# Kernel tuning notes

Measured on AMD Instinct MI355X. Metric: run time of the kernel, lower is better.

## Reference

```python
import jax, jax.numpy as jnp
import numpy as np

B, S, H = 2, 2048, 1024
NH, NKV, HD = 16, 4, 64
G, R = NKV, NH // NKV  # 4 kv groups, 4 query heads per group


def setup_inputs() -> dict:
    key = jax.random.key(0)
    ks = jax.random.split(key, 7)
    scale = 1.0 / np.sqrt(H)
    return {
        "hidden_states": jax.random.normal(ks[0], (B, S, H), jnp.float32),
        "cos": jax.random.normal(ks[1], (S, HD), jnp.float32),
        "sin": jax.random.normal(ks[2], (S, HD), jnp.float32),
        "attention_mask": jnp.ones((B, S), jnp.float32),
        "Wq": jax.random.normal(ks[3], (H, NH * HD), jnp.float32) * scale,
        "Wk": jax.random.normal(ks[4], (H, NKV * HD), jnp.float32) * scale,
        "Wv": jax.random.normal(ks[5], (H, NKV * HD), jnp.float32) * scale,
        "Wo": jax.random.normal(ks[6], (NH * HD, H), jnp.float32) * scale,
    }


def _rotate_half(x):
    h = x.shape[-1] // 2
    return jnp.concatenate([-x[..., h:], x[..., :h]], axis=-1)


def reference(hidden_states, cos, sin, attention_mask, Wq, Wk, Wv, Wo):
    x = hidden_states
    q = (x @ Wq).reshape(B, S, NH, HD)
    k = (x @ Wk).reshape(B, S, NKV, HD)
    v = (x @ Wv).reshape(B, S, NKV, HD)
    # RoPE: cos/sin [S,HD] broadcast over batch and heads
    c = cos[None, :, None, :]
    s = sin[None, :, None, :]
    q = q * c + _rotate_half(q) * s
    k = k * c + _rotate_half(k) * s
    # GQA without materializing repeated KV: q grouped as [B,S,G,R,HD]
    qg = q.reshape(B, S, G, R, HD)
    scores = jnp.einsum("bsgrd,btgd->bgrst", qg, k) / np.sqrt(HD)  # [B,G,R,S,T]
    causal = jnp.tril(jnp.ones((S, S), bool))
    scores = jnp.where(causal[None, None, None], scores, -jnp.inf)
    scores = scores + ((1.0 - attention_mask) * -1e9)[:, None, None, None, :]
    probs = jax.nn.softmax(scores.astype(jnp.float32), axis=-1).astype(q.dtype)
    out = jnp.einsum("bgrst,btgd->bsgrd", probs, v).reshape(B, S, NH * HD)
    return out @ Wo
```

## Files before the change

kernel.cpp:

```cpp
#include <hip/hip_runtime.h>
#include <math.h>

#define B_   2
#define S_   2048
#define H_   1024
#define NH_  16
#define NKV_ 4
#define HD_  64
#define R_   (NH_ / NKV_)
#define QKVW 1536

typedef __attribute__((ext_vector_type(8))) short bf16x8;
typedef __attribute__((ext_vector_type(4))) float f32x4;

__device__ inline short f2bf(float f) {
    unsigned u = __float_as_uint(f);
    u += 0x7FFF + ((u >> 16) & 1);
    return (short)(u >> 16);
}

__device__ inline void gload_lds16(const void* gptr, void* lptr) {
    __builtin_amdgcn_global_load_lds(
        (const __attribute__((address_space(1))) unsigned int*)gptr,
        (__attribute__((address_space(3))) unsigned int*)lptr,
        16, 0, 0);
}

__global__ __launch_bounds__(256) void tconv_all(const float* __restrict__ Wq,
                                                 const float* __restrict__ Wk,
                                                 const float* __restrict__ Wv,
                                                 const float* __restrict__ Wo,
                                                 short* __restrict__ Wqkvt,
                                                 short* __restrict__ Wot,
                                                 const float* __restrict__ x,
                                                 short* __restrict__ xb) {
    const int bx = blockIdx.x;
    const int tid = threadIdx.x;

    if (bx >= 640) {
        const size_t e0 = (size_t)(bx - 640) * 16384;
#pragma unroll
        for (int t = 0; t < 8; t++) {
            const size_t i = e0 + ((size_t)t * 256 + tid) * 8;
            float4 a = *(const float4*)&x[i];
            float4 c = *(const float4*)&x[i + 4];
            bf16x8 o;
            o[0] = f2bf(a.x); o[1] = f2bf(a.y); o[2] = f2bf(a.z); o[3] = f2bf(a.w);
            o[4] = f2bf(c.x); o[5] = f2bf(c.y); o[6] = f2bf(c.z); o[7] = f2bf(c.w);
            *(bf16x8*)&xb[i] = o;
        }
        return;
    }

    __shared__ short T[64][68];
    const float* W; short* Wt; int N, idx;
    if (bx < 256)      { W = Wq; Wt = Wqkvt;                     N = 1024; idx = bx; }
    else if (bx < 320) { W = Wk; Wt = Wqkvt + 1024 * 1024;       N = 256;  idx = bx - 256; }
    else if (bx < 384) { W = Wv; Wt = Wqkvt + 1280 * 1024;       N = 256;  idx = bx - 320; }
    else               { W = Wo; Wt = Wot;                       N = 1024; idx = bx - 384; }
    const int ntiles = N >> 6;
    const int n0 = (idx % ntiles) * 64;
    const int k0 = (idx / ntiles) * 64;

    const int r  = tid >> 4;
    const int c4 = (tid & 15) * 4;
#pragma unroll
    for (int t = 0; t < 4; t++) {
        int row = t * 16 + r;
        float4 v = *(const float4*)&W[(size_t)(k0 + row) * N + n0 + c4];
        T[c4 + 0][row] = f2bf(v.x);
        T[c4 + 1][row] = f2bf(v.y);
        T[c4 + 2][row] = f2bf(v.z);
        T[c4 + 3][row] = f2bf(v.w);
    }
    __syncthreads();
#pragma unroll
    for (int t = 0; t < 4; t++) {
        int row = t * 16 + r;
        short4 o = *(short4*)&T[row][c4];
        *(short4*)&Wt[(size_t)(n0 + row) * 1024 + k0 + c4] = o;
    }
}

__global__ __launch_bounds__(256) void gemm1_fused(const short* __restrict__ xb,
                                                   const short* __restrict__ Bt,
                                                   short* __restrict__ qkv,
                                                   short* __restrict__ Vtg,
                                                   const float* __restrict__ cosb,
                                                   const float* __restrict__ sinb) {
    __shared__ short Ah[128 * 32];
    __shared__ short Bh[128 * 32];

    const int tid  = threadIdx.x;
    const int w    = tid >> 6;
    const int lane = tid & 63;
    const int ln   = lane & 15;
    const int qd   = lane >> 4;
    const int wr   = w >> 1, wc = w & 1;
    const int row0 = blockIdx.y * 128;
    const int col0 = blockIdx.x * 128;

    const int sr = lane >> 2;
    const int sk = (lane & 3) * 8;

    f32x4 acc[4][4];
#pragma unroll
    for (int mi = 0; mi < 4; mi++)
#pragma unroll
        for (int ni = 0; ni < 4; ni++)
            acc[mi][ni] = (f32x4){0.f, 0.f, 0.f, 0.f};

    for (int k0 = 0; k0 < 1024; k0 += 32) {
        __syncthreads();
        gload_lds16(xb + (size_t)(row0 + w * 16 + sr) * 1024 + k0 + sk,      &Ah[(w * 16) * 32]);
        gload_lds16(xb + (size_t)(row0 + 64 + w * 16 + sr) * 1024 + k0 + sk, &Ah[(64 + w * 16) * 32]);
        gload_lds16(Bt + (size_t)(col0 + w * 16 + sr) * 1024 + k0 + sk,      &Bh[(w * 16) * 32]);
        gload_lds16(Bt + (size_t)(col0 + 64 + w * 16 + sr) * 1024 + k0 + sk, &Bh[(64 + w * 16) * 32]);
        __syncthreads();

        bf16x8 af[4], bf[4];
#pragma unroll
        for (int mi = 0; mi < 4; mi++)
            af[mi] = *(const bf16x8*)&Ah[(wr * 64 + mi * 16 + ln) * 32 + qd * 8];
#pragma unroll
        for (int ni = 0; ni < 4; ni++)
            bf[ni] = *(const bf16x8*)&Bh[(wc * 64 + ni * 16 + ln) * 32 + qd * 8];
#pragma unroll
        for (int mi = 0; mi < 4; mi++)
#pragma unroll
            for (int ni = 0; ni < 4; ni++)
                acc[mi][ni] = __builtin_amdgcn_mfma_f32_16x16x32_bf16(af[mi], bf[ni], acc[mi][ni], 0, 0, 0);
    }

    const int colw = col0 + wc * 64;
    if (colw < H_ + NKV_ * HD_) {
#pragma unroll
        for (int mi = 0; mi < 4; mi++)
#pragma unroll
            for (int i = 0; i < 4; i++) {
                const int row  = row0 + wr * 64 + mi * 16 + qd * 4 + i;
                const int spos = row & (S_ - 1);
                const float* cp = cosb + (size_t)spos * HD_;
                const float* sp = sinb + (size_t)spos * HD_;
                float o0[4];
#pragma unroll
                for (int ni = 0; ni < 2; ni++) {
                    const int d = ni * 16 + ln;
                    float x0 = acc[mi][ni][i], x1 = acc[mi][ni + 2][i];
                    o0[ni]     = x0 * cp[d]      - x1 * sp[d];
                    o0[ni + 2] = x1 * cp[d + 32] + x0 * sp[d + 32];
                }
                short* Cp = qkv + (size_t)row * QKVW + colw + ln;
#pragma unroll
                for (int ni = 0; ni < 4; ni++) Cp[ni * 16] = f2bf(o0[ni]);
            }
    } else {
        const int g = (colw - (H_ + NKV_ * HD_)) >> 6;
#pragma unroll
        for (int mi = 0; mi < 4; mi++) {
            const int rbase = row0 + wr * 64 + mi * 16 + qd * 4;
            const int bg = ((rbase >> 11) * NKV_) + g;
            const int s0 = rbase & (S_ - 1);
#pragma unroll
            for (int ni = 0; ni < 4; ni++) {
                const int d = ni * 16 + ln;
                short4 pk = { f2bf(acc[mi][ni][0]), f2bf(acc[mi][ni][1]),
                              f2bf(acc[mi][ni][2]), f2bf(acc[mi][ni][3]) };
                *(short4*)&Vtg[((size_t)bg * HD_ + d) * S_ + s0] = pk;
            }
        }
    }
}

__global__ __launch_bounds__(256) void gemm2_bt(const short* __restrict__ A, int lda,
                                                const short* __restrict__ Bt,
                                                float* __restrict__ C, int ldc,
                                                int K) {
    __shared__ short Ah[128 * 32];
    __shared__ short Bh[128 * 32];

    const int tid  = threadIdx.x;
    const int w    = tid >> 6;
    const int lane = tid & 63;
    const int ln   = lane & 15;
    const int qd   = lane >> 4;
    const int wr   = w >> 1, wc = w & 1;
    const int row0 = blockIdx.y * 128;
    const int col0 = blockIdx.x * 128;

    const int sr = lane >> 2;
    const int sk = (lane & 3) * 8;

    f32x4 acc[4][4];
#pragma unroll
    for (int mi = 0; mi < 4; mi++)
#pragma unroll
        for (int ni = 0; ni < 4; ni++)
            acc[mi][ni] = (f32x4){0.f, 0.f, 0.f, 0.f};

    for (int k0 = 0; k0 < K; k0 += 32) {
        __syncthreads();
        gload_lds16(A + (size_t)(row0 + w * 16 + sr) * lda + k0 + sk,      &Ah[(w * 16) * 32]);
        gload_lds16(A + (size_t)(row0 + 64 + w * 16 + sr) * lda + k0 + sk, &Ah[(64 + w * 16) * 32]);
        gload_lds16(Bt + (size_t)(col0 + w * 16 + sr) * K + k0 + sk,       &Bh[(w * 16) * 32]);
        gload_lds16(Bt + (size_t)(col0 + 64 + w * 16 + sr) * K + k0 + sk,  &Bh[(64 + w * 16) * 32]);
        __syncthreads();

        bf16x8 af[4], bf[4];
#pragma unroll
        for (int mi = 0; mi < 4; mi++)
            af[mi] = *(const bf16x8*)&Ah[(wr * 64 + mi * 16 + ln) * 32 + qd * 8];
#pragma unroll
        for (int ni = 0; ni < 4; ni++)
            bf[ni] = *(const bf16x8*)&Bh[(wc * 64 + ni * 16 + ln) * 32 + qd * 8];
#pragma unroll
        for (int mi = 0; mi < 4; mi++)
#pragma unroll
            for (int ni = 0; ni < 4; ni++)
                acc[mi][ni] = __builtin_amdgcn_mfma_f32_16x16x32_bf16(af[mi], bf[ni], acc[mi][ni], 0, 0, 0);
    }

#pragma unroll
    for (int mi = 0; mi < 4; mi++)
#pragma unroll
        for (int i = 0; i < 4; i++) {
            const size_t row = row0 + wr * 64 + mi * 16 + qd * 4 + i;
            float* Cp = C + row * ldc + col0 + wc * 64 + ln;
#pragma unroll
            for (int ni = 0; ni < 4; ni++) Cp[ni * 16] = acc[mi][ni][i];
        }
}

__global__ __launch_bounds__(512, 2) void attn_kernel(short* __restrict__ qkv,
                                                      const short* __restrict__ Vtg,
                                                      const float* __restrict__ maskb) {
    const int tid  = threadIdx.x;
    const int w    = tid >> 6;
    const int lane = tid & 63;
    const int ln   = lane & 15;
    const int qd   = lane >> 4;

    const int fid = blockIdx.x;
    const int bg  = fid & 7;
    const int u   = fid >> 3;
    const int b   = bg >> 2;
    const int g   = bg & 3;
    const int h   = g * R_ + (u & 3);
    const int a   = u >> 2;

    const int qt   = (w < 4) ? a : (15 - a);
    const int st   = w & 3;
    const int rowb = qt * 128 + st * 32;
    const int ktd  = 2 * qt + (st >> 1);
    const int nt   = 32 - 2 * a;

    __shared__ short Ks[2][64 * 72];
    __shared__ short Vt[2][64 * 72];
    __shared__ short Ps[8][16 * 72];
    __shared__ float mskS[2][64];
    short* const ps = Ps[w];

    const short* const Kb = qkv + (size_t)b * S_ * QKVW + H_ + g * HD_;
    const short* const Vb = Vtg + (size_t)bg * HD_ * S_;
    const float* const mb = maskb + b * S_;

    const int fr = tid >> 3;
    const int fc = (tid & 7) * 8;

    bf16x8 qf[2][2];
#pragma unroll
    for (int rg = 0; rg < 2; rg++) {
        const short* qp = qkv + (size_t)(b * S_ + rowb + rg * 16 + ln) * QKVW + h * HD_;
        qf[rg][0] = *(const bf16x8*)&qp[qd * 8];
        qf[rg][1] = *(const bf16x8*)&qp[32 + qd * 8];
    }

    f32x4 O[2][4] = {};
    float mrow[2] = {-1e30f, -1e30f};
    float lrow[2] = {0.0f, 0.0f};

    *(bf16x8*)&Ks[0][fr * 72 + fc] = *(const bf16x8*)&Kb[(size_t)fr * QKVW + fc];
    *(bf16x8*)&Vt[0][fr * 72 + fc] = *(const bf16x8*)&Vb[(size_t)fr * S_ + fc];
    if (tid < 64) mskS[0][tid] = mb[tid];
    __syncthreads();

    int cur = 0;
    for (int kt = 0; kt < nt; kt++) {
        const int base = kt * 64;
        const bool pf = (kt + 1 < nt);

        bf16x8 pk, pv;
        float pm = 0.0f;
        if (pf) {
            const int nb = base + 64;
            pk = *(const bf16x8*)&Kb[(size_t)(nb + fr) * QKVW + fc];
            pv = *(const bf16x8*)&Vb[(size_t)fr * S_ + nb + fc];
            if (tid < 64) pm = mb[nb + tid];
        }

        if (kt <= ktd) {
            f32x4 St[2][4];
#pragma unroll
            for (int kg = 0; kg < 4; kg++) {
                bf16x8 ka0 = *(const bf16x8*)&Ks[cur][(kg * 16 + ln) * 72 + qd * 8];
                bf16x8 ka1 = *(const bf16x8*)&Ks[cur][(kg * 16 + ln) * 72 + 32 + qd * 8];
#pragma unroll
                for (int rg = 0; rg < 2; rg++) {
                    f32x4 z = {0.f, 0.f, 0.f, 0.f};
                    z = __builtin_amdgcn_mfma_f32_16x16x32_bf16(ka0, qf[rg][0], z, 0, 0, 0);
                    St[rg][kg] = __builtin_amdgcn_mfma_f32_16x16x32_bf16(ka1, qf[rg][1], z, 0, 0, 0);
                }
            }

            bf16x8 vb[2][4];
#pragma unroll
            for (int kc2 = 0; kc2 < 2; kc2++)
#pragma unroll
                for (int dt = 0; dt < 4; dt++)
                    vb[kc2][dt] = *(const bf16x8*)&Vt[cur][(dt * 16 + ln) * 72 + kc2 * 32 + qd * 8];

            float mt[4][4];
#pragma unroll
            for (int kg = 0; kg < 4; kg++) {
                float4 mv = *(const float4*)&mskS[cur][kg * 16 + qd * 4];
                mt[kg][0] = (1.0f - mv.x) * -1e9f;
                mt[kg][1] = (1.0f - mv.y) * -1e9f;
                mt[kg][2] = (1.0f - mv.z) * -1e9f;
                mt[kg][3] = (1.0f - mv.w) * -1e9f;
            }

            const bool diag = (kt == ktd);

#pragma unroll
            for (int rg = 0; rg < 2; rg++) {
                const int qrow = rowb + rg * 16 + ln;
                float sc[4][4];
#pragma unroll
                for (int kg = 0; kg < 4; kg++) {
                    const int keyb = base + kg * 16 + qd * 4;
#pragma unroll
                    for (int i = 0; i < 4; i++) {
                        float v = fmaf(St[rg][kg][i], 0.125f, mt[kg][i]);
                        sc[kg][i] = (diag && (keyb + i > qrow)) ? -1e30f : v;
                    }
                }
                float mx = sc[0][0];
#pragma unroll
                for (int kg = 0; kg < 4; kg++)
#pragma unroll
                    for (int i = 0; i < 4; i++) mx = fmaxf(mx, sc[kg][i]);
                mx = fmaxf(mx, __shfl_xor(mx, 16));
                mx = fmaxf(mx, __shfl_xor(mx, 32));

                if (__ballot(mx > mrow[rg] + 8.0f)) {
                    float nm    = fmaxf(mrow[rg], mx);
                    float alpha = __expf(mrow[rg] - nm);
                    lrow[rg] *= alpha;
#pragma unroll
                    for (int i = 0; i < 4; i++) {
                        float av = __shfl(alpha, qd * 4 + i);
#pragma unroll
                        for (int dt = 0; dt < 4; dt++) O[rg][dt][i] *= av;
                    }
                    mrow[rg] = nm;
                }
                const float nm = mrow[rg];

                float ls = 0.0f;
#pragma unroll
                for (int kg = 0; kg < 4; kg++)
#pragma unroll
                    for (int i = 0; i < 4; i++) {
                        float p = __expf(sc[kg][i] - nm);
                        sc[kg][i] = p;
                        ls += p;
                    }
                ls += __shfl_xor(ls, 16);
                ls += __shfl_xor(ls, 32);
                lrow[rg] += ls;

#pragma unroll
                for (int kg = 0; kg < 4; kg++) {
                    short4 pk2 = { f2bf(sc[kg][0]), f2bf(sc[kg][1]),
                                   f2bf(sc[kg][2]), f2bf(sc[kg][3]) };
                    *(short4*)&ps[ln * 72 + kg * 16 + qd * 4] = pk2;
                }

#pragma unroll
                for (int kc2 = 0; kc2 < 2; kc2++) {
                    bf16x8 pa = *(const bf16x8*)&ps[ln * 72 + kc2 * 32 + qd * 8];
#pragma unroll
                    for (int dt = 0; dt < 4; dt++)
                        O[rg][dt] = __builtin_amdgcn_mfma_f32_16x16x32_bf16(pa, vb[kc2][dt], O[rg][dt], 0, 0, 0);
                }
            }
        }

        if (pf) {
            const int nxt = cur ^ 1;
            *(bf16x8*)&Ks[nxt][fr * 72 + fc] = pk;
            *(bf16x8*)&Vt[nxt][fr * 72 + fc] = pv;
            if (tid < 64) mskS[nxt][tid] = pm;
        }
        __syncthreads();
        cur ^= 1;
    }

#pragma unroll
    for (int rg = 0; rg < 2; rg++)
#pragma unroll
        for (int i = 0; i < 4; i++) {
            float li  = __shfl(lrow[rg], qd * 4 + i);
            float inv = 1.0f / li;
            const int row = rowb + rg * 16 + qd * 4 + i;
            short* op = qkv + (size_t)(b * S_ + row) * QKVW + h * HD_ + ln;
#pragma unroll
            for (int dt = 0; dt < 4; dt++) op[dt * 16] = f2bf(O[rg][dt][i] * inv);
        }
}

extern "C" void kernel_launch(void* const* d_in, const int* in_sizes, int n_in,
                              void* d_out, int out_size, void* d_ws, size_t ws_size,
                              hipStream_t stream) {
    const float* x     = (const float*)d_in[0];
    const float* cosb  = (const float*)d_in[1];
    const float* sinb  = (const float*)d_in[2];
    const float* maskb = (const float*)d_in[3];
    const float* Wq    = (const float*)d_in[4];
    const float* Wk    = (const float*)d_in[5];
    const float* Wv    = (const float*)d_in[6];
    const float* Wo    = (const float*)d_in[7];

    const int M = B_ * S_;

    short* qkv   = (short*)d_ws;
    short* Wqkvt = qkv + (size_t)M * QKVW;
    short* Wot   = Wqkvt + (size_t)QKVW * H_;
    short* Vtg   = Wot + (size_t)H_ * H_;
    short* xb    = (short*)d_out;
    float* out   = (float*)d_out;

    dim3 blk(256);

    tconv_all<<<dim3(896), blk, 0, stream>>>(Wq, Wk, Wv, Wo, Wqkvt, Wot, x, xb);

    gemm1_fused<<<dim3(QKVW / 128, M / 128), blk, 0, stream>>>(xb, Wqkvt, qkv, Vtg, cosb, sinb);

    attn_kernel<<<dim3(256), dim3(512), 0, stream>>>(qkv, Vtg, maskb);

    gemm2_bt<<<dim3(H_ / 128, M / 128), blk, 0, stream>>>(qkv, QKVW, Wot, out, H_, H_);
}
```

Before: 206.6 us.

## Process paired causal query tiles sequentially with all eight waves per tile

Before, each block split its eight waves into two groups, each handling a different query tile (a and 15-a) with 32 rows per wave, streaming K/V once across the longer range. Now all eight waves handle 16 rows each of one tile, then the block moves to the paired tile in a second phase, so each phase only streams the K/V range its tile needs. The mask transform is also precomputed when loading into shared memory. This halves per-wave register state and removes idle iterations for the short tile, but reloads K/V for the overlapping prefix and adds a second pipeline prologue and more barriers.

```diff
diff --git a/kernel.cpp b/kernel.cpp
--- a/kernel.cpp
+++ b/kernel.cpp
@@ -248,12 +248,6 @@
     const int h   = g * R_ + (u & 3);
     const int a   = u >> 2;
 
-    const int qt   = (w < 4) ? a : (15 - a);
-    const int st   = w & 3;
-    const int rowb = qt * 128 + st * 32;
-    const int ktd  = 2 * qt + (st >> 1);
-    const int nt   = 32 - 2 * a;
-
     __shared__ short Ks[2][64 * 72];
     __shared__ short Vt[2][64 * 72];
     __shared__ short Ps[8][16 * 72];
@@ -267,83 +261,81 @@
     const int fr = tid >> 3;
     const int fc = (tid & 7) * 8;
 
-    bf16x8 qf[2][2];
-#pragma unroll
-    for (int rg = 0; rg < 2; rg++) {
-        const short* qp = qkv + (size_t)(b * S_ + rowb + rg * 16 + ln) * QKVW + h * HD_;
-        qf[rg][0] = *(const bf16x8*)&qp[qd * 8];
-        qf[rg][1] = *(const bf16x8*)&qp[32 + qd * 8];
-    }
-
-    f32x4 O[2][4] = {};
-    float mrow[2] = {-1e30f, -1e30f};
-    float lrow[2] = {0.0f, 0.0f};
-
-    *(bf16x8*)&Ks[0][fr * 72 + fc] = *(const bf16x8*)&Kb[(size_t)fr * QKVW + fc];
-    *(bf16x8*)&Vt[0][fr * 72 + fc] = *(const bf16x8*)&Vb[(size_t)fr * S_ + fc];
-    if (tid < 64) mskS[0][tid] = mb[tid];
-    __syncthreads();
-
-    int cur = 0;
-    for (int kt = 0; kt < nt; kt++) {
-        const int base = kt * 64;
-        const bool pf = (kt + 1 < nt);
-
-        bf16x8 pk, pv;
-        float pm = 0.0f;
-        if (pf) {
-            const int nb = base + 64;
-            pk = *(const bf16x8*)&Kb[(size_t)(nb + fr) * QKVW + fc];
-            pv = *(const bf16x8*)&Vb[(size_t)fr * S_ + nb + fc];
-            if (tid < 64) pm = mb[nb + tid];
-        }
-
-        if (kt <= ktd) {
-            f32x4 St[2][4];
-#pragma unroll
-            for (int kg = 0; kg < 4; kg++) {
-                bf16x8 ka0 = *(const bf16x8*)&Ks[cur][(kg * 16 + ln) * 72 + qd * 8];
-                bf16x8 ka1 = *(const bf16x8*)&Ks[cur][(kg * 16 + ln) * 72 + 32 + qd * 8];
-#pragma unroll
-                for (int rg = 0; rg < 2; rg++) {
+#pragma unroll 1
+    for (int ph = 0; ph < 2; ph++) {
+        const int qt   = ph ? (15 - a) : a;
+        const int rowb = qt * 128 + w * 16;
+        const int ktd  = 2 * qt + (w >> 2);
+        const int ntp  = 2 * qt + 2;
+        const int qrow = rowb + ln;
+
+        bf16x8 qf0, qf1;
+        {
+            const short* qp = qkv + (size_t)(b * S_ + rowb + ln) * QKVW + h * HD_;
+            qf0 = *(const bf16x8*)&qp[qd * 8];
+            qf1 = *(const bf16x8*)&qp[32 + qd * 8];
+        }
+
+        f32x4 O[4] = {};
+        float mrow = -1e30f, lrow = 0.0f;
+
+        *(bf16x8*)&Ks[0][fr * 72 + fc] = *(const bf16x8*)&Kb[(size_t)fr * QKVW + fc];
+        *(bf16x8*)&Vt[0][fr * 72 + fc] = *(const bf16x8*)&Vb[(size_t)fr * S_ + fc];
+        if (tid < 64) mskS[0][tid] = (1.0f - mb[tid]) * -1e9f;
+        __syncthreads();
+
+        int cur = 0;
+#pragma unroll 1
+        for (int kt = 0; kt < ntp; kt++) {
+            const int base = kt * 64;
+            const bool pf = (kt + 1 < ntp);
+
+            bf16x8 pk, pv;
+            float pm = 0.0f;
+            if (pf) {
+                const int nb = base + 64;
+                pk = *(const bf16x8*)&Kb[(size_t)(nb + fr) * QKVW + fc];
+                pv = *(const bf16x8*)&Vb[(size_t)fr * S_ + nb + fc];
+                if (tid < 64) pm = (1.0f - mb[nb + tid]) * -1e9f;
+            }
+
+            if (kt <= ktd) {
+                f32x4 St[4];
+#pragma unroll
+                for (int kg = 0; kg < 4; kg++) {
+                    bf16x8 ka0 = *(const bf16x8*)&Ks[cur][(kg * 16 + ln) * 72 + qd * 8];
+                    bf16x8 ka1 = *(const bf16x8*)&Ks[cur][(kg * 16 + ln) * 72 + 32 + qd * 8];
                     f32x4 z = {0.f, 0.f, 0.f, 0.f};
-                    z = __builtin_amdgcn_mfma_f32_16x16x32_bf16(ka0, qf[rg][0], z, 0, 0, 0);
-                    St[rg][kg] = __builtin_amdgcn_mfma_f32_16x16x32_bf16(ka1, qf[rg][1], z, 0, 0, 0);
-                }
-            }
-
-            bf16x8 vb[2][4];
-#pragma unroll
-            for (int kc2 = 0; kc2 < 2; kc2++)
-#pragma unroll
-                for (int dt = 0; dt < 4; dt++)
-                    vb[kc2][dt] = *(const bf16x8*)&Vt[cur][(dt * 16 + ln) * 72 + kc2 * 32 + qd * 8];
-
-            float mt[4][4];
-#pragma unroll
-            for (int kg = 0; kg < 4; kg++) {
-                float4 mv = *(const float4*)&mskS[cur][kg * 16 + qd * 4];
-                mt[kg][0] = (1.0f - mv.x) * -1e9f;
-                mt[kg][1] = (1.0f - mv.y) * -1e9f;
-                mt[kg][2] = (1.0f - mv.z) * -1e9f;
-                mt[kg][3] = (1.0f - mv.w) * -1e9f;
-            }
-
-            const bool diag = (kt == ktd);
-
-#pragma unroll
-            for (int rg = 0; rg < 2; rg++) {
-                const int qrow = rowb + rg * 16 + ln;
+                    z = __builtin_amdgcn_mfma_f32_16x16x32_bf16(ka0, qf0, z, 0, 0, 0);
+                    St[kg] = __builtin_amdgcn_mfma_f32_16x16x32_bf16(ka1, qf1, z, 0, 0, 0);
+                }
+
+                bf16x8 vb[2][4];
+#pragma unroll
+                for (int kc2 = 0; kc2 < 2; kc2++)
+#pragma unroll
+                    for (int dt = 0; dt < 4; dt++)
+                        vb[kc2][dt] = *(const bf16x8*)&Vt[cur][(dt * 16 + ln) * 72 + kc2 * 32 + qd * 8];
+
                 float sc[4][4];
 #pragma unroll
                 for (int kg = 0; kg < 4; kg++) {
-                    const int keyb = base + kg * 16 + qd * 4;
-#pragma unroll
-                    for (int i = 0; i < 4; i++) {
-                        float v = fmaf(St[rg][kg][i], 0.125f, mt[kg][i]);
-                        sc[kg][i] = (diag && (keyb + i > qrow)) ? -1e30f : v;
+                    float4 mv = *(const float4*)&mskS[cur][kg * 16 + qd * 4];
+                    sc[kg][0] = fmaf(St[kg][0], 0.125f, mv.x);
+                    sc[kg][1] = fmaf(St[kg][1], 0.125f, mv.y);
+                    sc[kg][2] = fmaf(St[kg][2], 0.125f, mv.z);
+                    sc[kg][3] = fmaf(St[kg][3], 0.125f, mv.w);
+                }
+                if (kt == ktd) {
+#pragma unroll
+                    for (int kg = 0; kg < 4; kg++) {
+                        const int keyb = base + kg * 16 + qd * 4;
+#pragma unroll
+                        for (int i = 0; i < 4; i++)
+                            if (keyb + i > qrow) sc[kg][i] = -1e30f;
                     }
                 }
+
                 float mx = sc[0][0];
 #pragma unroll
                 for (int kg = 0; kg < 4; kg++)
@@ -352,19 +344,19 @@
                 mx = fmaxf(mx, __shfl_xor(mx, 16));
                 mx = fmaxf(mx, __shfl_xor(mx, 32));
 
-                if (__ballot(mx > mrow[rg] + 8.0f)) {
-                    float nm    = fmaxf(mrow[rg], mx);
-                    float alpha = __expf(mrow[rg] - nm);
-                    lrow[rg] *= alpha;
+                if (__ballot(mx > mrow + 8.0f)) {
+                    float nm    = fmaxf(mrow, mx);
+                    float alpha = __expf(mrow - nm);
+                    lrow *= alpha;
 #pragma unroll
                     for (int i = 0; i < 4; i++) {
                         float av = __shfl(alpha, qd * 4 + i);
 #pragma unroll
-                        for (int dt = 0; dt < 4; dt++) O[rg][dt][i] *= av;
+                        for (int dt = 0; dt < 4; dt++) O[dt][i] *= av;
                     }
-                    mrow[rg] = nm;
-                }
-                const float nm = mrow[rg];
+                    mrow = nm;
+                }
+                const float nm = mrow;
 
                 float ls = 0.0f;
 #pragma unroll
@@ -377,13 +369,13 @@
                     }
                 ls += __shfl_xor(ls, 16);
                 ls += __shfl_xor(ls, 32);
-                lrow[rg] += ls;
+                lrow += ls;
 
 #pragma unroll
                 for (int kg = 0; kg < 4; kg++) {
-                    short4 pk2 = { f2bf(sc[kg][0]), f2bf(sc[kg][1]),
+                    short4 pko = { f2bf(sc[kg][0]), f2bf(sc[kg][1]),
                                    f2bf(sc[kg][2]), f2bf(sc[kg][3]) };
-                    *(short4*)&ps[ln * 72 + kg * 16 + qd * 4] = pk2;
+                    *(short4*)&ps[ln * 72 + kg * 16 + qd * 4] = pko;
                 }
 
 #pragma unroll
@@ -391,32 +383,30 @@
                     bf16x8 pa = *(const bf16x8*)&ps[ln * 72 + kc2 * 32 + qd * 8];
 #pragma unroll
                     for (int dt = 0; dt < 4; dt++)
-                        O[rg][dt] = __builtin_amdgcn_mfma_f32_16x16x32_bf16(pa, vb[kc2][dt], O[rg][dt], 0, 0, 0);
+                        O[dt] = __builtin_amdgcn_mfma_f32_16x16x32_bf16(pa, vb[kc2][dt], O[dt], 0, 0, 0);
                 }
             }
-        }
-
-        if (pf) {
-            const int nxt = cur ^ 1;
-            *(bf16x8*)&Ks[nxt][fr * 72 + fc] = pk;
-            *(bf16x8*)&Vt[nxt][fr * 72 + fc] = pv;
-            if (tid < 64) mskS[nxt][tid] = pm;
-        }
-        __syncthreads();
-        cur ^= 1;
-    }
-
-#pragma unroll
-    for (int rg = 0; rg < 2; rg++)
+
+            if (pf) {
+                const int nxt = cur ^ 1;
+                *(bf16x8*)&Ks[nxt][fr * 72 + fc] = pk;
+                *(bf16x8*)&Vt[nxt][fr * 72 + fc] = pv;
+                if (tid < 64) mskS[nxt][tid] = pm;
+            }
+            __syncthreads();
+            cur ^= 1;
+        }
+
 #pragma unroll
         for (int i = 0; i < 4; i++) {
-            float li  = __shfl(lrow[rg], qd * 4 + i);
+            float li  = __shfl(lrow, qd * 4 + i);
             float inv = 1.0f / li;
-            const int row = rowb + rg * 16 + qd * 4 + i;
+            const int row = rowb + qd * 4 + i;
             short* op = qkv + (size_t)(b * S_ + row) * QKVW + h * HD_ + ln;
 #pragma unroll
-            for (int dt = 0; dt < 4; dt++) op[dt * 16] = f2bf(O[rg][dt][i] * inv);
-        }
+            for (int dt = 0; dt < 4; dt++) op[dt * 16] = f2bf(O[dt][i] * inv);
+        }
+    }
 }
 
 extern "C" void kernel_launch(void* const* d_in, const int* in_sizes, int n_in,
```

After: 195.0 us. 5.6% less time.
